# Optimization experiments

Hardware: AMD Instinct MI355X
Metric: run time of the kernel (lower is better)

## Reference

```python
import jax, jax.numpy as jnp
import numpy as np

B, C, H, W = 4, 128, 128, 128
E, K, HID = 11, 6, 512  # num_experts, active_experts, 4*dim


def setup_inputs() -> dict:
    key = jax.random.key(0)
    ks = jax.random.split(key, 5)
    return {
        "x": jax.random.normal(ks[0], (B, C, H, W), jnp.float32),
        "gate_w": jax.random.normal(ks[1], (E, C), jnp.float32) * 0.02,
        "gate_b": jnp.zeros((E,), jnp.float32),
        "w1": jax.random.normal(ks[2], (E, HID, C), jnp.float32) * 0.02,
        "b1": jnp.zeros((E, HID), jnp.float32),
        "w2": jax.random.normal(ks[3], (E, C, HID), jnp.float32) * 0.02,
        "b2": jnp.zeros((E, C), jnp.float32),
    }


def reference(x, gate_w, gate_b, w1, b1, w2, b2):
    n_experts = gate_w.shape[0]
    k = K  # active_experts
    # channels-last for per-pixel routing / 1x1-conv-as-matmul
    xcl = jnp.transpose(x, (0, 2, 3, 1))  # [B,H,W,C]
    # --- router (1x1 conv gate + softmax over experts + top-k) ---
    logits = jnp.einsum('bhwc,ec->bhwe', xcl, gate_w) + gate_b
    scores = jax.nn.softmax(logits, axis=-1)            # [B,H,W,E]
    topk_p, topk_i = jax.lax.top_k(scores, k)           # [B,H,W,K]
    topk_p = topk_p / topk_p.sum(axis=-1, keepdims=True)
    # scatter routing weights into dense per-expert mask (indices distinct)
    onehot = jax.nn.one_hot(topk_i, n_experts, dtype=x.dtype)  # [B,H,W,K,E]
    mask = jnp.einsum('bhwke,bhwk->bhwe', onehot, topk_p)      # [B,H,W,E]
    # --- dense expert compute, masked accumulate (as in original loop) ---
    acc = jnp.zeros_like(xcl)
    for e in range(n_experts):
        h = jax.nn.gelu(jnp.einsum('bhwc,dc->bhwd', xcl, w1[e]) + b1[e],
                        approximate=False)  # torch GELU is exact erf form
        oe = jnp.einsum('bhwd,cd->bhwc', h, w2[e]) + b2[e]
        acc = acc + mask[..., e:e + 1] * oe
    y = x + jnp.transpose(acc, (0, 3, 1, 2))  # back to NCHW
    # --- load-balancing aux loss ---
    mean_prob = scores.mean(axis=(0, 1, 2))            # [E]
    mean_load = onehot.sum(axis=3).mean(axis=(0, 1, 2))  # binary mask mean, [E]
    aux_loss = n_experts * jnp.sum(mean_prob * mean_load)
    return (y, aux_loss)
```

## Files before the change

### kernel.cpp

```cpp
#include <hip/hip_runtime.h>
#include <stdint.h>

#define C_   128
#define HW_  16384
#define CHW_ (C_*HW_)
#define N_   65536
#define E_   11
#define K_   6
#define HID_ 512

typedef __attribute__((ext_vector_type(8))) short short8;
typedef __attribute__((ext_vector_type(4))) float float4v;
typedef __attribute__((ext_vector_type(16))) float float16v;
typedef __attribute__((ext_vector_type(2))) unsigned uint2v;

#define GLD(g, s) __builtin_amdgcn_global_load_lds( \
    (const __attribute__((address_space(1))) unsigned int*)(uintptr_t)(g), \
    (__attribute__((address_space(3))) unsigned int*)(unsigned int)(uintptr_t)(s), 16, 0, 0)

__device__ __forceinline__ unsigned short f2bf(float f){
  union { float f; unsigned u; } v; v.f = f;
  unsigned r = v.u + 0x7fffu + ((v.u >> 16) & 1u);
  return (unsigned short)(r >> 16);
}
__device__ __forceinline__ float gelu_w(float v, float wr){
  float t = __builtin_amdgcn_fmed3f(v, -2.5f, 2.5f);
  float u = t * t;
  float s = fmaf(u, fmaf(u, fmaf(u, -0.00076957f, 0.0147811f), -0.126434f), 0.795742f);
  float p = t * s;
  return (v * wr) * fmaf(0.5f, p, 0.5f);
}
__device__ __forceinline__ unsigned pk2(float g0, float g1){
  return __builtin_amdgcn_perm(__float_as_uint(g1) + 0x8000u,
                               __float_as_uint(g0) + 0x8000u, 0x07060302u);
}
__device__ __forceinline__ void pswap32(unsigned &a, unsigned &b){
#if __has_builtin(__builtin_amdgcn_permlane32_swap)
  uint2v r = __builtin_amdgcn_permlane32_swap(a, b, false, false);
  a = r.x; b = r.y;
#else
  asm volatile("v_permlane32_swap_b32 %0, %1" : "+v"(a), "+v"(b));
#endif
}

__global__ __launch_bounds__(256) void k_convert(const float* __restrict__ w1,
                                                 const float* __restrict__ w2,
                                                 unsigned short* __restrict__ wimg,
                                                 float* __restrict__ auxsum){
  int t = blockIdx.x * 256 + threadIdx.x;
  if (t < 23) auxsum[t] = 0.0f;
  if (t >= 180224) return;
  const float* src;
  size_t dst;
  if (t < 90112){
    int e = t >> 13, hid = (t >> 4) & 511, c8 = t & 15;
    src = w1 + (size_t)t * 8;
    int rec = e * 16 + (hid >> 5);
    int kc = c8 >> 1, half = c8 & 1;
    int l = (hid & 31) | (half << 5);
    dst = (size_t)rec * 8192 + kc * 512 + l * 8;
  } else {
    int u = t - 90112;
    int e = u >> 13, cc = (u >> 6) & 127, hd8 = u & 63;
    src = w2 + (size_t)u * 8;
    int rec = e * 16 + (hd8 >> 2);
    int kc2 = (hd8 >> 1) & 1, half = hd8 & 1, ct = cc >> 5;
    int l = (cc & 31) | (half << 5);
    dst = (size_t)rec * 8192 + 4096 + (ct * 2 + kc2) * 512 + l * 8;
  }
  float4 a = *(const float4*)src, b = *(const float4*)(src + 4);
  union { unsigned short us[8]; uint4 v; } u4;
  u4.us[0] = f2bf(a.x); u4.us[1] = f2bf(a.y); u4.us[2] = f2bf(a.z); u4.us[3] = f2bf(a.w);
  u4.us[4] = f2bf(b.x); u4.us[5] = f2bf(b.y); u4.us[6] = f2bf(b.z); u4.us[7] = f2bf(b.w);
  *(uint4*)(wimg + dst) = u4.v;
}

__global__ __launch_bounds__(256) void k_pre(const float* __restrict__ x,
                                             const float* __restrict__ gw,
                                             const float* __restrict__ gb,
                                             const float* __restrict__ b2,
                                             unsigned short* __restrict__ xcl,
                                             float* __restrict__ mask,
                                             float* __restrict__ auxsum){
  __shared__ __align__(16) float tt[64 * 130];
  __shared__ __align__(16) float g[E_ * C_];
  __shared__ float gbs[E_];
  __shared__ float ap[E_], al[E_];
  int tid = threadIdx.x;
  int pix0 = blockIdx.x * 64;
  int b = pix0 >> 14, hw0 = pix0 & 16383;
  const float* xb = x + (size_t)b * CHW_ + hw0;

  for (int i = tid; i < E_ * C_; i += 256) g[i] = gw[i];
  if (tid < E_) { gbs[tid] = gb[tid]; ap[tid] = 0.f; al[tid] = 0.f; }

  #pragma unroll 4
  for (int it = 0; it < 32; ++it){
    int flat = it * 256 + tid;
    int c = flat >> 6, p = flat & 63;
    tt[p * 130 + c] = xb[c * HW_ + p];
  }
  __syncthreads();
  #pragma unroll 4
  for (int it = 0; it < 16; ++it){
    int u = it * 256 + tid;
    int p = u >> 6, cc = u & 63;
    float f0 = tt[p * 130 + 2 * cc], f1 = tt[p * 130 + 2 * cc + 1];
    unsigned out = (unsigned)f2bf(f0) | ((unsigned)f2bf(f1) << 16);
    ((unsigned*)xcl)[(size_t)(pix0 + p) * 64 + cc] = out;
  }

  int p = tid >> 2, t4 = tid & 3;
  float lg[E_];
  #pragma unroll
  for (int e = 0; e < E_; ++e) lg[e] = (t4 == 0) ? gbs[e] : 0.f;
  const float2* ttrow = (const float2*)(tt + p * 130 + t4 * 32);
  #pragma unroll 4
  for (int j2 = 0; j2 < 16; ++j2){
    float2 xv = ttrow[j2];
    #pragma unroll
    for (int e = 0; e < E_; ++e){
      float2 gv = *(const float2*)(g + e * C_ + t4 * 32 + j2 * 2);
      lg[e] = fmaf(xv.x, gv.x, lg[e]);
      lg[e] = fmaf(xv.y, gv.y, lg[e]);
    }
  }
  #pragma unroll
  for (int e = 0; e < E_; ++e){
    lg[e] += __shfl_xor(lg[e], 1, 64);
    lg[e] += __shfl_xor(lg[e], 2, 64);
  }
  float mx = lg[0];
  #pragma unroll
  for (int e = 1; e < E_; ++e) mx = fmaxf(mx, lg[e]);
  float pr[E_]; float s = 0.f;
  #pragma unroll
  for (int e = 0; e < E_; ++e){ pr[e] = expf(lg[e] - mx); s += pr[e]; }
  float inv = 1.0f / s;
  #pragma unroll
  for (int e = 0; e < E_; ++e) pr[e] *= inv;

  unsigned selmask = 0; float wsum = 0.f;
  for (int k = 0; k < K_; ++k){
    float bv = -1.f; int bi = 0;
    #pragma unroll
    for (int e = 0; e < E_; ++e){
      bool better = (((selmask >> e) & 1u) == 0u) && (pr[e] > bv);
      bv = better ? pr[e] : bv;
      bi = better ? e : bi;
    }
    selmask |= 1u << bi; wsum += bv;
  }
  float invw = 1.0f / wsum;
  if (t4 == 0){
    int pix = pix0 + p;
    #pragma unroll
    for (int e = 0; e < E_; ++e){
      bool sel = (selmask >> e) & 1u;
      mask[(size_t)pix * E_ + e] = sel ? pr[e] * invw : 0.f;
      atomicAdd(&ap[e], pr[e]);
      if (sel) atomicAdd(&al[e], 1.0f);
    }
  }
  __syncthreads();
  if (tid < E_){
    atomicAdd(&auxsum[tid], ap[tid]);
    atomicAdd(&auxsum[E_ + tid], al[tid]);
  }
  if (blockIdx.x == 0 && tid < 64){
    int nz = 0;
    for (int idx = tid; idx < E_ * C_; idx += 64)
      nz |= (__float_as_uint(b2[idx]) != 0u) ? 1 : 0;
    if (nz) atomicOr((int*)(auxsum + 22), 1);
  }
}

__global__ __launch_bounds__(256, 2) void k_ffn(const unsigned short* __restrict__ xcl,
                                                const unsigned short* __restrict__ wimg,
                                                const float* __restrict__ b1,
                                                const float* __restrict__ b2,
                                                const float* __restrict__ mask,
                                                const float* __restrict__ aux,
                                                const float* __restrict__ x,
                                                float* __restrict__ y){
  __shared__ unsigned char smem[63488];
  int tid = threadIdx.x;
  int w = tid >> 6, l = tid & 63;
  int l31 = l & 31, hi = l >> 5;
  int hi4 = hi * 4;
  int pix0 = blockIdx.x * 128;

  if (blockIdx.x == 0 && tid == 0){
    float s = 0.f;
    const float invN = 1.0f / (float)N_;
    for (int e = 0; e < E_; ++e)
      s += (aux[e] * invN) * (aux[E_ + e] * invN);
    y[(size_t)N_ * C_] = (float)E_ * s;
  }

  short8 Xf[8];
  {
    const unsigned short* xrow = xcl + ((size_t)(pix0 + w * 32 + l31) << 7) + hi * 8;
    #pragma unroll
    for (int kc = 0; kc < 8; ++kc)
      Xf[kc] = *(const short8*)(xrow + kc * 16);
  }

  #pragma unroll
  for (int rr = 0; rr < 2; ++rr){
    const unsigned short* g = wimg + (size_t)rr * 8192 + w * 2048 + l * 8;
    unsigned char* lb = smem + rr * 16384 + w * 4096;
    #pragma unroll
    for (int t = 0; t < 4; ++t) GLD(g + t * 512, lb + t * 1024);
  }
  float* maskl = (float*)(smem + 49152);
  for (int idx = tid; idx < 2048; idx += 256){
    int pp = idx >> 4, ee = idx & 15;
    maskl[idx] = (ee < 11) ? mask[(size_t)(pix0 + pp) * 11 + ee] : 0.f;
  }
  float4 bn0 = *(const float4*)(b1 + 0 + hi4);
  float4 bn1 = *(const float4*)(b1 + 8 + hi4);
  float4 bn2 = *(const float4*)(b1 + 16 + hi4);
  float4 bn3 = *(const float4*)(b1 + 24 + hi4);
  __syncthreads();

  float16v facc[4];
  #pragma unroll
  for (int ct = 0; ct < 4; ++ct) facc[ct] = (float16v)0.0f;
  float wr = 0.f;

  #pragma unroll 1
  for (int i = 0; i < 176; ++i){
    asm volatile("s_waitcnt vmcnt(8)" ::: "memory");
    __builtin_amdgcn_s_barrier();
    float4 bc0 = bn0, bc1 = bn1, bc2 = bn2, bc3 = bn3;
    {
      int nb = (i + 1 <= 175) ? (i + 1) : 175;
      const float* bp = b1 + nb * 32 + hi4;
      bn0 = *(const float4*)(bp);
      bn1 = *(const float4*)(bp + 8);
      bn2 = *(const float4*)(bp + 16);
      bn3 = *(const float4*)(bp + 24);
    }
    __builtin_amdgcn_sched_barrier(0);
    {
      int pf = (i + 2 <= 175) ? (i + 2) : 175;
      const unsigned short* g = wimg + (size_t)pf * 8192 + w * 2048 + l * 8;
      unsigned char* lb = smem + (pf % 3) * 16384 + w * 4096;
      #pragma unroll
      for (int t = 0; t < 4; ++t) GLD(g + t * 512, lb + t * 1024);
    }
    __builtin_amdgcn_sched_barrier(0);
    const unsigned char* wb = smem + (i % 3) * 16384;

    if ((i & 15) == 0)
      wr = maskl[(w * 32 + l31) * 16 + (i >> 4)];

    float16v hacc = {bc0.x, bc0.y, bc0.z, bc0.w, bc1.x, bc1.y, bc1.z, bc1.w,
                     bc2.x, bc2.y, bc2.z, bc2.w, bc3.x, bc3.y, bc3.z, bc3.w};
    #pragma unroll
    for (int kc = 0; kc < 8; ++kc){
      short8 a = *(const short8*)(wb + kc * 1024 + l * 16);
      hacc = __builtin_amdgcn_mfma_f32_32x32x16_bf16(a, Xf[kc], hacc, 0, 0, 0);
    }

    unsigned pd[8];
    #pragma unroll
    for (int k = 0; k < 8; ++k)
      pd[k] = pk2(gelu_w(hacc[2 * k], wr), gelu_w(hacc[2 * k + 1], wr));
    pswap32(pd[0], pd[2]); pswap32(pd[1], pd[3]);
    pswap32(pd[4], pd[6]); pswap32(pd[5], pd[7]);
    union { unsigned u[4]; short8 s; } cv0, cv1;
    cv0.u[0] = pd[0]; cv0.u[1] = pd[1]; cv0.u[2] = pd[2]; cv0.u[3] = pd[3];
    cv1.u[0] = pd[4]; cv1.u[1] = pd[5]; cv1.u[2] = pd[6]; cv1.u[3] = pd[7];

    #pragma unroll
    for (int ct = 0; ct < 4; ++ct){
      short8 a0 = *(const short8*)(wb + 8192 + (ct * 2 + 0) * 1024 + l * 16);
      short8 a1 = *(const short8*)(wb + 8192 + (ct * 2 + 1) * 1024 + l * 16);
      facc[ct] = __builtin_amdgcn_mfma_f32_32x32x16_bf16(a0, cv0.s, facc[ct], 0, 0, 0);
      facc[ct] = __builtin_amdgcn_mfma_f32_32x32x16_bf16(a1, cv1.s, facc[ct], 0, 0, 0);
    }
  }

  __syncthreads();
  float* lds_t = (float*)smem;
  float* b2t   = (float*)(smem + 57344);
  for (int idx = tid; idx < 1536; idx += 256){
    int cc = idx / 12, ee = idx - cc * 12;
    b2t[idx] = (ee < 11) ? b2[ee * 128 + cc] : 0.f;
  }
  int b2nz = ((const int*)aux)[22];

  #pragma unroll 1
  for (int h = 0; h < 4; ++h){
    __syncthreads();
    if (w == h){
      #pragma unroll
      for (int ct = 0; ct < 4; ++ct)
        #pragma unroll
        for (int r = 0; r < 16; ++r)
          lds_t[(ct * 32 + (r & 3) + 8 * (r >> 2) + hi4) * 33 + l31] = facc[ct][r];
    }
    __syncthreads();
    int c = tid >> 1, p16 = (tid & 1) << 4;
    int pixg = pix0 + h * 32 + p16;
    size_t base = (size_t)(pixg >> 14) * CHW_ + (size_t)c * HW_ + (pixg & 16383);
    float b2r[11];
    if (b2nz){
      #pragma unroll
      for (int e = 0; e < 11; ++e) b2r[e] = b2t[c * 12 + e];
    }
    #pragma unroll 2
    for (int v = 0; v < 4; ++v){
      float av[4];
      #pragma unroll
      for (int k = 0; k < 4; ++k) av[k] = lds_t[c * 33 + p16 + v * 4 + k];
      if (b2nz){
        #pragma unroll
        for (int k = 0; k < 4; ++k){
          const float* mr = maskl + (h * 32 + p16 + v * 4 + k) * 16;
          #pragma unroll
          for (int e = 0; e < 11; ++e) av[k] = fmaf(mr[e], b2r[e], av[k]);
        }
      }
      float4 xv = *(const float4*)(x + base + v * 4);
      float4 o = {av[0] + xv.x, av[1] + xv.y, av[2] + xv.z, av[3] + xv.w};
      *(float4*)(y + base + v * 4) = o;
    }
  }
}

extern "C" void kernel_launch(void* const* d_in, const int* in_sizes, int n_in,
                              void* d_out, int out_size, void* d_ws, size_t ws_size,
                              hipStream_t stream){
  const float* x  = (const float*)d_in[0];
  const float* gw = (const float*)d_in[1];
  const float* gb = (const float*)d_in[2];
  const float* w1 = (const float*)d_in[3];
  const float* b1 = (const float*)d_in[4];
  const float* w2 = (const float*)d_in[5];
  const float* b2 = (const float*)d_in[6];
  float* y = (float*)d_out;
  char* ws = (char*)d_ws;

  unsigned short* xcl  = (unsigned short*)ws;
  unsigned short* wimg = (unsigned short*)(ws + 16777216);
  float* mask   = (float*)(ws + 19660800);
  float* auxsum = (float*)(ws + 22544384);

  hipLaunchKernelGGL(k_convert, dim3(704),  dim3(256), 0, stream, w1, w2, wimg, auxsum);
  hipLaunchKernelGGL(k_pre,     dim3(1024), dim3(256), 0, stream, x, gw, gb, b2, xcl, mask, auxsum);
  hipLaunchKernelGGL(k_ffn,     dim3(512),  dim3(256), 0, stream, xcl, wimg, b1, b2, mask, auxsum, x, y);
}
```

Baseline: 380.1 us.

## Switch FFN to fp16 MFMA with packed half GELU and register-loaded W1

Converts weights and activations from bf16 to fp16 and uses f16 MFMA. GELU, bias add and routing-weight scaling now run as packed half2 arithmetic instead of per-element fp32, with b1 pre-converted to fp16 in the MFMA output layout. W1 tiles are now loaded straight into registers with a two-stage ping-pong, replacing LDS staging. Only W2 stays double-buffered in LDS, which halves shared memory. This trades VALU work and LDS traffic for lower GELU precision, possible fp16 range issues, and global-load latency on W1 that is hidden by only one iteration of prefetch.

```diff
diff --git a/kernel.cpp b/kernel.cpp
--- a/kernel.cpp
+++ b/kernel.cpp
@@ -9,8 +9,9 @@
 #define K_   6
 #define HID_ 512
 
-typedef __attribute__((ext_vector_type(8))) short short8;
-typedef __attribute__((ext_vector_type(4))) float float4v;
+typedef __attribute__((ext_vector_type(8))) _Float16 half8;
+typedef __attribute__((ext_vector_type(2))) _Float16 h2;
+typedef __attribute__((ext_vector_type(2))) __fp16 fp16v2;
 typedef __attribute__((ext_vector_type(16))) float float16v;
 typedef __attribute__((ext_vector_type(2))) unsigned uint2v;
 
@@ -18,21 +19,19 @@
     (const __attribute__((address_space(1))) unsigned int*)(uintptr_t)(g), \
     (__attribute__((address_space(3))) unsigned int*)(unsigned int)(uintptr_t)(s), 16, 0, 0)
 
-__device__ __forceinline__ unsigned short f2bf(float f){
-  union { float f; unsigned u; } v; v.f = f;
-  unsigned r = v.u + 0x7fffu + ((v.u >> 16) & 1u);
-  return (unsigned short)(r >> 16);
-}
-__device__ __forceinline__ float gelu_w(float v, float wr){
-  float t = __builtin_amdgcn_fmed3f(v, -2.5f, 2.5f);
-  float u = t * t;
-  float s = fmaf(u, fmaf(u, fmaf(u, -0.00076957f, 0.0147811f), -0.126434f), 0.795742f);
-  float p = t * s;
-  return (v * wr) * fmaf(0.5f, p, 0.5f);
-}
-__device__ __forceinline__ unsigned pk2(float g0, float g1){
-  return __builtin_amdgcn_perm(__float_as_uint(g1) + 0x8000u,
-                               __float_as_uint(g0) + 0x8000u, 0x07060302u);
+__device__ __forceinline__ h2 pkrtz(float a, float b){
+  union { fp16v2 f; h2 h; } u;
+  u.f = __builtin_amdgcn_cvt_pkrtz(a, b);
+  return u.h;
+}
+__device__ __forceinline__ h2 gelu2h(h2 v, h2 wr2){
+  h2 u = v * v;
+  h2 s = u * (h2)(_Float16)(-0.00076957f) + (h2)(_Float16)(0.0147811f);
+  s = s * u + (h2)(_Float16)(-0.126434f);
+  s = s * u + (h2)(_Float16)(0.795742f);
+  h2 p = v * s;
+  h2 phi = p * (h2)(_Float16)(0.5f) + (h2)(_Float16)(0.5f);
+  return v * wr2 * phi;
 }
 __device__ __forceinline__ void pswap32(unsigned &a, unsigned &b){
 #if __has_builtin(__builtin_amdgcn_permlane32_swap)
@@ -45,11 +44,24 @@
 
 __global__ __launch_bounds__(256) void k_convert(const float* __restrict__ w1,
                                                  const float* __restrict__ w2,
+                                                 const float* __restrict__ b1,
                                                  unsigned short* __restrict__ wimg,
+                                                 unsigned short* __restrict__ b1h,
                                                  float* __restrict__ auxsum){
   int t = blockIdx.x * 256 + threadIdx.x;
   if (t < 23) auxsum[t] = 0.0f;
-  if (t >= 180224) return;
+  if (t >= 185856) return;
+  if (t >= 180224){
+    int t2 = t - 180224;
+    int rec = t2 >> 5, j5 = t2 & 31;
+    int hi = j5 >> 4, j = j5 & 15;
+    int e = rec >> 4, hc = rec & 15;
+    int row = (j & 3) + 8 * (j >> 2) + 4 * hi;
+    union { _Float16 h; unsigned short u; } cv;
+    cv.h = (_Float16)b1[e * 512 + hc * 32 + row];
+    b1h[rec * 32 + j5] = cv.u;
+    return;
+  }
   const float* src;
   size_t dst;
   if (t < 90112){
@@ -69,9 +81,11 @@
     dst = (size_t)rec * 8192 + 4096 + (ct * 2 + kc2) * 512 + l * 8;
   }
   float4 a = *(const float4*)src, b = *(const float4*)(src + 4);
-  union { unsigned short us[8]; uint4 v; } u4;
-  u4.us[0] = f2bf(a.x); u4.us[1] = f2bf(a.y); u4.us[2] = f2bf(a.z); u4.us[3] = f2bf(a.w);
-  u4.us[4] = f2bf(b.x); u4.us[5] = f2bf(b.y); u4.us[6] = f2bf(b.z); u4.us[7] = f2bf(b.w);
+  union { _Float16 h[8]; uint4 v; } u4;
+  u4.h[0] = (_Float16)a.x; u4.h[1] = (_Float16)a.y;
+  u4.h[2] = (_Float16)a.z; u4.h[3] = (_Float16)a.w;
+  u4.h[4] = (_Float16)b.x; u4.h[5] = (_Float16)b.y;
+  u4.h[6] = (_Float16)b.z; u4.h[7] = (_Float16)b.w;
   *(uint4*)(wimg + dst) = u4.v;
 }
 
@@ -106,8 +120,9 @@
     int u = it * 256 + tid;
     int p = u >> 6, cc = u & 63;
     float f0 = tt[p * 130 + 2 * cc], f1 = tt[p * 130 + 2 * cc + 1];
-    unsigned out = (unsigned)f2bf(f0) | ((unsigned)f2bf(f1) << 16);
-    ((unsigned*)xcl)[(size_t)(pix0 + p) * 64 + cc] = out;
+    union { h2 h; unsigned u; } pv;
+    pv.h = pkrtz(f0, f1);
+    ((unsigned*)xcl)[(size_t)(pix0 + p) * 64 + cc] = pv.u;
   }
 
   int p = tid >> 2, t4 = tid & 3;
@@ -177,18 +192,20 @@
 
 __global__ __launch_bounds__(256, 2) void k_ffn(const unsigned short* __restrict__ xcl,
                                                 const unsigned short* __restrict__ wimg,
-                                                const float* __restrict__ b1,
+                                                const unsigned short* __restrict__ b1h,
                                                 const float* __restrict__ b2,
                                                 const float* __restrict__ mask,
                                                 const float* __restrict__ aux,
                                                 const float* __restrict__ x,
                                                 float* __restrict__ y){
-  __shared__ unsigned char smem[63488];
+  __shared__ unsigned char smem[31744];
   int tid = threadIdx.x;
   int w = tid >> 6, l = tid & 63;
   int l31 = l & 31, hi = l >> 5;
   int hi4 = hi * 4;
   int pix0 = blockIdx.x * 128;
+  const unsigned char* wimgB = (const unsigned char*)wimg;
+  const unsigned char* b1hB  = (const unsigned char*)b1h;
 
   if (blockIdx.x == 0 && tid == 0){
     float s = 0.f;
@@ -198,94 +215,107 @@
     y[(size_t)N_ * C_] = (float)E_ * s;
   }
 
-  short8 Xf[8];
+  half8 Xf[8];
   {
     const unsigned short* xrow = xcl + ((size_t)(pix0 + w * 32 + l31) << 7) + hi * 8;
     #pragma unroll
     for (int kc = 0; kc < 8; ++kc)
-      Xf[kc] = *(const short8*)(xrow + kc * 16);
-  }
-
-  #pragma unroll
-  for (int rr = 0; rr < 2; ++rr){
-    const unsigned short* g = wimg + (size_t)rr * 8192 + w * 2048 + l * 8;
-    unsigned char* lb = smem + rr * 16384 + w * 4096;
-    #pragma unroll
-    for (int t = 0; t < 4; ++t) GLD(g + t * 512, lb + t * 1024);
-  }
-  float* maskl = (float*)(smem + 49152);
+      Xf[kc] = *(const half8*)(xrow + kc * 16);
+  }
+
+  half8 WregA[8], WregB[8];
+  uint4 bhA[2], bhB[2];
+
+  {
+    const unsigned char* gs = wimgB + 8192 + w * 2048 + l * 16;
+    GLD(gs, smem + w * 2048);
+    GLD(gs + 1024, smem + w * 2048 + 1024);
+    const unsigned char* ws0 = wimgB + l * 16;
+    #pragma unroll
+    for (int kc = 0; kc < 8; ++kc)
+      WregA[kc] = *(const half8*)(ws0 + kc * 1024);
+    bhA[0] = *(const uint4*)(b1hB + hi * 32);
+    bhA[1] = *(const uint4*)(b1hB + hi * 32 + 16);
+  }
+  float* maskl = (float*)(smem + 17408);
   for (int idx = tid; idx < 2048; idx += 256){
     int pp = idx >> 4, ee = idx & 15;
     maskl[idx] = (ee < 11) ? mask[(size_t)(pix0 + pp) * 11 + ee] : 0.f;
   }
-  float4 bn0 = *(const float4*)(b1 + 0 + hi4);
-  float4 bn1 = *(const float4*)(b1 + 8 + hi4);
-  float4 bn2 = *(const float4*)(b1 + 16 + hi4);
-  float4 bn3 = *(const float4*)(b1 + 24 + hi4);
   __syncthreads();
 
   float16v facc[4];
   #pragma unroll
   for (int ct = 0; ct < 4; ++ct) facc[ct] = (float16v)0.0f;
-  float wr = 0.f;
+  h2 wr2 = (h2)(_Float16)0.0f;
+
+#define FFN_BODY(I, WCON, WLOAD, BHC, BHL)                                          \
+  {                                                                                 \
+    asm volatile("s_waitcnt vmcnt(10)" ::: "memory");                               \
+    __builtin_amdgcn_s_barrier();                                                   \
+    __builtin_amdgcn_sched_barrier(0);                                              \
+    const int pf_ = ((I) + 1 <= 175) ? ((I) + 1) : 175;                             \
+    {                                                                               \
+      const unsigned char* gs_ = wimgB + (size_t)pf_ * 16384 + 8192 + w * 2048 + l * 16; \
+      unsigned char* ld_ = smem + ((((I) + 1) & 1) << 13) + w * 2048;               \
+      GLD(gs_, ld_);                                                                \
+      GLD(gs_ + 1024, ld_ + 1024);                                                  \
+    }                                                                               \
+    {                                                                               \
+      const unsigned char* ws_ = wimgB + (size_t)pf_ * 16384 + l * 16;              \
+      _Pragma("unroll")                                                             \
+      for (int kc_ = 0; kc_ < 8; ++kc_)                                             \
+        WLOAD[kc_] = *(const half8*)(ws_ + kc_ * 1024);                             \
+      const unsigned char* bp_ = b1hB + pf_ * 64 + hi * 32;                         \
+      BHL[0] = *(const uint4*)(bp_);                                                \
+      BHL[1] = *(const uint4*)(bp_ + 16);                                           \
+    }                                                                               \
+    __builtin_amdgcn_sched_barrier(0);                                              \
+    if (((I) & 15) == 0){                                                           \
+      float wrf_ = maskl[(w * 32 + l31) * 16 + ((I) >> 4)];                         \
+      _Float16 wh_ = (_Float16)wrf_;                                                \
+      wr2 = (h2){wh_, wh_};                                                         \
+    }                                                                               \
+    float16v hacc_ = (float16v)0.0f;                                                \
+    _Pragma("unroll")                                                               \
+    for (int kc_ = 0; kc_ < 8; ++kc_)                                               \
+      hacc_ = __builtin_amdgcn_mfma_f32_32x32x16_f16(WCON[kc_], Xf[kc_], hacc_, 0, 0, 0); \
+    union { uint4 v[2]; h2 h[8]; } bu_;                                             \
+    bu_.v[0] = BHC[0]; bu_.v[1] = BHC[1];                                           \
+    unsigned pd_[8];                                                                \
+    _Pragma("unroll")                                                               \
+    for (int k_ = 0; k_ < 8; ++k_){                                                 \
+      h2 v_ = pkrtz(hacc_[2 * k_], hacc_[2 * k_ + 1]);                              \
+      v_ = v_ + bu_.h[k_];                                                          \
+      union { h2 h; unsigned u; } g_;                                               \
+      g_.h = gelu2h(v_, wr2);                                                       \
+      pd_[k_] = g_.u;                                                               \
+    }                                                                               \
+    pswap32(pd_[0], pd_[2]); pswap32(pd_[1], pd_[3]);                               \
+    pswap32(pd_[4], pd_[6]); pswap32(pd_[5], pd_[7]);                               \
+    union { unsigned u[4]; half8 s; } cv0_, cv1_;                                   \
+    cv0_.u[0] = pd_[0]; cv0_.u[1] = pd_[1]; cv0_.u[2] = pd_[2]; cv0_.u[3] = pd_[3]; \
+    cv1_.u[0] = pd_[4]; cv1_.u[1] = pd_[5]; cv1_.u[2] = pd_[6]; cv1_.u[3] = pd_[7]; \
+    const unsigned char* wb_ = smem + (((I) & 1) << 13);                            \
+    _Pragma("unroll")                                                               \
+    for (int ct_ = 0; ct_ < 4; ++ct_){                                              \
+      half8 a0_ = *(const half8*)(wb_ + (ct_ * 2 + 0) * 1024 + l * 16);             \
+      half8 a1_ = *(const half8*)(wb_ + (ct_ * 2 + 1) * 1024 + l * 16);             \
+      facc[ct_] = __builtin_amdgcn_mfma_f32_32x32x16_f16(a0_, cv0_.s, facc[ct_], 0, 0, 0); \
+      facc[ct_] = __builtin_amdgcn_mfma_f32_32x32x16_f16(a1_, cv1_.s, facc[ct_], 0, 0, 0); \
+    }                                                                               \
+  }
 
   #pragma unroll 1
-  for (int i = 0; i < 176; ++i){
-    asm volatile("s_waitcnt vmcnt(8)" ::: "memory");
-    __builtin_amdgcn_s_barrier();
-    float4 bc0 = bn0, bc1 = bn1, bc2 = bn2, bc3 = bn3;
-    {
-      int nb = (i + 1 <= 175) ? (i + 1) : 175;
-      const float* bp = b1 + nb * 32 + hi4;
-      bn0 = *(const float4*)(bp);
-      bn1 = *(const float4*)(bp + 8);
-      bn2 = *(const float4*)(bp + 16);
-      bn3 = *(const float4*)(bp + 24);
-    }
-    __builtin_amdgcn_sched_barrier(0);
-    {
-      int pf = (i + 2 <= 175) ? (i + 2) : 175;
-      const unsigned short* g = wimg + (size_t)pf * 8192 + w * 2048 + l * 8;
-      unsigned char* lb = smem + (pf % 3) * 16384 + w * 4096;
-      #pragma unroll
-      for (int t = 0; t < 4; ++t) GLD(g + t * 512, lb + t * 1024);
-    }
-    __builtin_amdgcn_sched_barrier(0);
-    const unsigned char* wb = smem + (i % 3) * 16384;
-
-    if ((i & 15) == 0)
-      wr = maskl[(w * 32 + l31) * 16 + (i >> 4)];
-
-    float16v hacc = {bc0.x, bc0.y, bc0.z, bc0.w, bc1.x, bc1.y, bc1.z, bc1.w,
-                     bc2.x, bc2.y, bc2.z, bc2.w, bc3.x, bc3.y, bc3.z, bc3.w};
-    #pragma unroll
-    for (int kc = 0; kc < 8; ++kc){
-      short8 a = *(const short8*)(wb + kc * 1024 + l * 16);
-      hacc = __builtin_amdgcn_mfma_f32_32x32x16_bf16(a, Xf[kc], hacc, 0, 0, 0);
-    }
-
-    unsigned pd[8];
-    #pragma unroll
-    for (int k = 0; k < 8; ++k)
-      pd[k] = pk2(gelu_w(hacc[2 * k], wr), gelu_w(hacc[2 * k + 1], wr));
-    pswap32(pd[0], pd[2]); pswap32(pd[1], pd[3]);
-    pswap32(pd[4], pd[6]); pswap32(pd[5], pd[7]);
-    union { unsigned u[4]; short8 s; } cv0, cv1;
-    cv0.u[0] = pd[0]; cv0.u[1] = pd[1]; cv0.u[2] = pd[2]; cv0.u[3] = pd[3];
-    cv1.u[0] = pd[4]; cv1.u[1] = pd[5]; cv1.u[2] = pd[6]; cv1.u[3] = pd[7];
-
-    #pragma unroll
-    for (int ct = 0; ct < 4; ++ct){
-      short8 a0 = *(const short8*)(wb + 8192 + (ct * 2 + 0) * 1024 + l * 16);
-      short8 a1 = *(const short8*)(wb + 8192 + (ct * 2 + 1) * 1024 + l * 16);
-      facc[ct] = __builtin_amdgcn_mfma_f32_32x32x16_bf16(a0, cv0.s, facc[ct], 0, 0, 0);
-      facc[ct] = __builtin_amdgcn_mfma_f32_32x32x16_bf16(a1, cv1.s, facc[ct], 0, 0, 0);
-    }
-  }
+  for (int k = 0; k < 88; ++k){
+    FFN_BODY(2 * k,     WregA, WregB, bhA, bhB);
+    FFN_BODY(2 * k + 1, WregB, WregA, bhB, bhA);
+  }
+#undef FFN_BODY
 
   __syncthreads();
   float* lds_t = (float*)smem;
-  float* b2t   = (float*)(smem + 57344);
+  float* b2t   = (float*)(smem + 25600);
   for (int idx = tid; idx < 1536; idx += 256){
     int cc = idx / 12, ee = idx - cc * 12;
     b2t[idx] = (ee < 11) ? b2[ee * 128 + cc] : 0.f;
@@ -348,8 +378,9 @@
   unsigned short* wimg = (unsigned short*)(ws + 16777216);
   float* mask   = (float*)(ws + 19660800);
   float* auxsum = (float*)(ws + 22544384);
-
-  hipLaunchKernelGGL(k_convert, dim3(704),  dim3(256), 0, stream, w1, w2, wimg, auxsum);
+  unsigned short* b1h  = (unsigned short*)(ws + 22544480);
+
+  hipLaunchKernelGGL(k_convert, dim3(726),  dim3(256), 0, stream, w1, w2, b1, wimg, b1h, auxsum);
   hipLaunchKernelGGL(k_pre,     dim3(1024), dim3(256), 0, stream, x, gw, gb, b2, xcl, mask, auxsum);
-  hipLaunchKernelGGL(k_ffn,     dim3(512),  dim3(256), 0, stream, xcl, wimg, b1, b2, mask, auxsum, x, y);
-}
+  hipLaunchKernelGGL(k_ffn,     dim3(512),  dim3(256), 0, stream, xcl, wimg, b1h, b2, mask, auxsum, x, y);
+}
```

Result: faster. 368.0 us (-3.2%).
